# Performance work log

Measured on AMD Instinct MI355X. Metric: run time of the kernel, lower is better.

## Reference

```python
import jax, jax.numpy as jnp
import numpy as np

B, C, L, D, H = 8, 64, 128, 768, 768  # batch, candidates, tokens, hidden, mlp hidden


def setup_inputs() -> dict:
    key = jax.random.key(0)
    k0, k1, k2 = jax.random.split(key, 3)
    inp = jax.random.normal(k0, (B, C, 2, L, D), dtype=jnp.float32)
    # MlpModule params (input_size = 768*2): Linear(2D->H) -> ReLU -> Linear(H->1)
    W1 = jax.random.normal(k1, (2 * D, H), dtype=jnp.float32) * 0.02
    b1 = jnp.zeros((H,), dtype=jnp.float32)
    W2 = jax.random.normal(k2, (H, 1), dtype=jnp.float32) * 0.02
    b2 = jnp.zeros((1,), dtype=jnp.float32)
    return {"input": inp, "W1": W1, "b1": b1, "W2": W2, "b2": b2}


def reference(input, W1, b1, W2, b2):
    b, c, _, l, d = input.shape
    context = input[:, :, 0].reshape(b * c, l, d)  # [BC, L, D]
    entity = input[:, :, 1].reshape(b * c, l, d)   # [BC, L, D]
    mask = (context[:, :, 0] != 0).astype(context.dtype)  # [BC, L]

    # bmm similarity: [BC, L, L]
    sim = jnp.einsum('bld,bmd->blm', context, entity)
    dot_scores = jnp.max(sim, axis=-1)          # [BC, L]
    argmax_values = jnp.argmax(sim, axis=-1)    # [BC, L]

    # gather best-matching entity token per context token: [BC, L, D]
    gathered = jnp.take_along_axis(entity, argmax_values[..., None], axis=1)

    # MLP over stacked (context, entity) pair -> flatten to 2D features
    mlp_in = jnp.concatenate([context, gathered], axis=-1)  # [BC, L, 2D]
    h = jax.nn.relu(mlp_in @ W1 + b1)
    scores = (h @ W2 + b2)[..., 0]              # [BC, L]

    scores = jnp.sum(scores * mask, axis=-1)              # [BC]
    dot_scores = jnp.sum(dot_scores * mask, axis=-1).reshape(b, c)  # [B, C]
    return scores, dot_scores
```

## Files before the change

### kernel.cpp

```cpp
#include <hip/hip_runtime.h>
#include <hip/hip_bf16.h>
#include <stdint.h>

#define NPAIR 512
#define LTOK  128
#define DDIM  768
#define HDIM  768
#define K2    1536
#define MARGIN 0.4f

typedef float f32x4 __attribute__((ext_vector_type(4)));
typedef short bf16x8 __attribute__((ext_vector_type(8)));

static __device__ __forceinline__ int fsw(int row) {
    return (row ^ (row >> 2)) & 3;
}

static __device__ __forceinline__ unsigned short f2bf(float f) {
    union { float f; uint32_t u; } v; v.f = f;
    uint32_t u = v.u;
    u += 0x7FFF + ((u >> 16) & 1);
    return (unsigned short)(u >> 16);
}

static __device__ __forceinline__ uint2 pack4(f32x4 v) {
    __hip_bfloat162 lo = __float22bfloat162_rn(float2{v[0], v[1]});
    __hip_bfloat162 hi = __float22bfloat162_rn(float2{v[2], v[3]});
    uint2 r;
    r.x = *reinterpret_cast<unsigned*>(&lo);
    r.y = *reinterpret_cast<unsigned*>(&hi);
    return r;
}

static __device__ __forceinline__ uint4 pack8(f32x4 a, f32x4 b) {
    uint2 lo = pack4(a), hi = pack4(b);
    uint4 r; r.x = lo.x; r.y = lo.y; r.z = hi.x; r.w = hi.y;
    return r;
}

typedef const __attribute__((address_space(1))) void* gas_t;
typedef __attribute__((address_space(3))) void* las_t;
static __device__ __forceinline__ void gld16(const void* g, void* l) {
    __builtin_amdgcn_global_load_lds((gas_t)g, (las_t)l, 16, 0, 0);
}

static __device__ __forceinline__ float wave_dot(const float* __restrict__ a,
                                                 const float* __restrict__ b,
                                                 int lane) {
    f32x4 s4 = {0.f, 0.f, 0.f, 0.f};
#pragma unroll
    for (int it = 0; it < 3; ++it) {
        int k = it * 256 + lane * 4;
        f32x4 av = *(const f32x4*)(a + k);
        f32x4 bv = *(const f32x4*)(b + k);
#pragma unroll
        for (int q = 0; q < 4; ++q) s4[q] = fmaf(av[q], bv[q], s4[q]);
    }
    float v = (s4[0] + s4[1]) + (s4[2] + s4[3]);
#pragma unroll
    for (int m = 1; m < 64; m <<= 1) v += __shfl_xor(v, m);
    return v;
}

__global__ __launch_bounds__(256, 2) void simfma_kernel(
        const float* __restrict__ inp,
        float* __restrict__ dotmax, int* __restrict__ argmax,
        unsigned short* __restrict__ Cbf, unsigned short* __restrict__ Ebf)
{
    const int p    = blockIdx.x;
    const int t    = threadIdx.x;
    const int wv   = t >> 6;
    const int lane = t & 63;
    const int s    = lane & 15, g = lane >> 4;

    const float* Cbase = inp + (size_t)(2 * p) * LTOK * DDIM;
    const float* Ebase = Cbase + (size_t)LTOK * DDIM;

    __shared__ unsigned short Cl[2][128][32];
    __shared__ unsigned short El[2][128][32];
    __shared__ unsigned short cand[128][16];
    __shared__ int   ccnt[128];
    __shared__ float rm1[128];
    __shared__ int   ri1[128];

    if (t < 128) ccnt[t] = 0;

    f32x4 acc[2][8];
#pragma unroll
    for (int i = 0; i < 2; i++)
#pragma unroll
        for (int j = 0; j < 8; j++) acc[i][j] = (f32x4){0.f, 0.f, 0.f, 0.f};

    const int srow[4] = { (0*256 + t) >> 3, (1*256 + t) >> 3,
                          (2*256 + t) >> 3, (3*256 + t) >> 3 };
    const int so8 = t & 7;
    const int sh  = so8 >> 2;
    const int sq  = so8 & 3;

    f32x4 cbuf[8], ebuf[8];

    auto ISSUE = [&](int kc) {
        const int k0 = kc * 64;
#pragma unroll
        for (int it = 0; it < 4; ++it) {
            const float* ca = Cbase + (size_t)srow[it] * DDIM + k0 + so8 * 8;
            const float* ea = Ebase + (size_t)srow[it] * DDIM + k0 + so8 * 8;
            cbuf[it * 2]     = *(const f32x4*)ca;
            cbuf[it * 2 + 1] = *(const f32x4*)(ca + 4);
            ebuf[it * 2]     = *(const f32x4*)ea;
            ebuf[it * 2 + 1] = *(const f32x4*)(ea + 4);
        }
    };

    ISSUE(0);
    for (int kc = 0; kc < 12; ++kc) {
        const int k0 = kc * 64;
        uint4 cw[4], ew[4];
#pragma unroll
        for (int it = 0; it < 4; ++it) {
            cw[it] = pack8(cbuf[it * 2], cbuf[it * 2 + 1]);
            ew[it] = pack8(ebuf[it * 2], ebuf[it * 2 + 1]);
            const int qs = (sq ^ fsw(srow[it])) * 8;
            *(uint4*)&Cl[sh][srow[it]][qs] = cw[it];
            *(uint4*)&El[sh][srow[it]][qs] = ew[it];
        }
        __syncthreads();

        if (kc < 11) ISSUE(kc + 1);
#pragma unroll
        for (int it = 0; it < 4; ++it) {
            size_t off = ((size_t)p * LTOK + srow[it]) * DDIM + k0 + so8 * 8;
            *(uint4*)(Cbf + off) = cw[it];
            *(uint4*)(Ebf + off) = ew[it];
        }

#pragma unroll
        for (int h = 0; h < 2; ++h) {
            bf16x8 af[2], bfr[8];
#pragma unroll
            for (int i = 0; i < 2; ++i) {
                const int row = wv * 32 + i * 16 + s;
                af[i] = *(const bf16x8*)&Cl[h][row][(g ^ fsw(row)) * 8];
            }
#pragma unroll
            for (int j = 0; j < 8; ++j) {
                const int row = j * 16 + s;
                bfr[j] = *(const bf16x8*)&El[h][row][(g ^ fsw(row)) * 8];
            }
#pragma unroll
            for (int i = 0; i < 2; ++i)
#pragma unroll
                for (int j = 0; j < 8; ++j)
                    acc[i][j] = __builtin_amdgcn_mfma_f32_16x16x32_bf16(af[i], bfr[j], acc[i][j], 0, 0, 0);
        }
        __syncthreads();
    }

#pragma unroll
    for (int i = 0; i < 2; ++i)
#pragma unroll
        for (int r = 0; r < 4; ++r) {
            float m1 = acc[i][0][r]; int i1 = s; float m2 = -1e30f;
#pragma unroll
            for (int j = 1; j < 8; ++j) {
                float v = acc[i][j][r]; int c = j * 16 + s;
                if (v > m1 || (v == m1 && c < i1)) { m2 = m1; m1 = v; i1 = c; }
                else if (v > m2) m2 = v;
            }
#pragma unroll
            for (int msk = 1; msk < 16; msk <<= 1) {
                float o1 = __shfl_xor(m1, msk);
                int   oi = __shfl_xor(i1, msk);
                float o2 = __shfl_xor(m2, msk);
                bool take = (o1 > m1) || (o1 == m1 && oi < i1);
                float nm2 = take ? fmaxf(m1, o2) : fmaxf(m2, o1);
                if (take) { m1 = o1; i1 = oi; }
                m2 = nm2;
            }
            int row = wv * 32 + i * 16 + g * 4 + r;
            if (s == 0) { rm1[row] = m1; ri1[row] = i1; }
            float thr = m1 - MARGIN;
#pragma unroll
            for (int j = 0; j < 8; ++j) {
                float v = acc[i][j][r]; int c = j * 16 + s;
                if (v >= thr && c != i1) {
                    int idx = atomicAdd(&ccnt[row], 1);
                    if (idx < 16) cand[row][idx] = (unsigned short)c;
                }
            }
        }
    __syncthreads();

    for (int rr = 0; rr < 32; ++rr) {
        int row = wv + rr * 4;
        int cnt = ccnt[row];
        float m1 = rm1[row]; int i1 = ri1[row];
        size_t ob = (size_t)p * LTOK + row;
        if (cnt == 0) {
            if (lane == 0) { dotmax[ob] = m1; argmax[ob] = i1; }
            continue;
        }
        const float* cr = Cbase + (size_t)row * DDIM;
        float bv; int bc;
        if (cnt <= 16) {
            bv = wave_dot(cr, Ebase + (size_t)i1 * DDIM, lane); bc = i1;
            for (int q = 0; q < cnt; ++q) {
                int c = cand[row][q];
                float v = wave_dot(cr, Ebase + (size_t)c * DDIM, lane);
                if (v > bv || (v == bv && c < bc)) { bv = v; bc = c; }
            }
        } else {
            bv = -1e30f; bc = 0;
            for (int c = 0; c < 128; ++c) {
                float v = wave_dot(cr, Ebase + (size_t)c * DDIM, lane);
                if (v > bv || (v == bv && c < bc)) { bv = v; bc = c; }
            }
        }
        if (lane == 0) { dotmax[ob] = bv; argmax[ob] = bc; }
    }
}

__global__ __launch_bounds__(256) void w1t_kernel(
        const float* __restrict__ W1, unsigned short* __restrict__ W1T)
{
    int idx = blockIdx.x * 256 + threadIdx.x;
    if (idx >= HDIM * K2 / 8) return;
    int c  = idx / (K2 / 8);
    int k0 = (idx % (K2 / 8)) * 8;
    unsigned short v[8];
#pragma unroll
    for (int q = 0; q < 8; q++) v[q] = f2bf(W1[(size_t)(k0 + q) * HDIM + c]);
    *(uint4*)(W1T + (size_t)c * K2 + k0) = *(const uint4*)v;
}

__global__ __launch_bounds__(256, 2) void mlp2_kernel(
        const unsigned short* __restrict__ Cbf,
        const unsigned short* __restrict__ Ebf,
        const unsigned short* __restrict__ W1T,
        const float* __restrict__ b1,
        const float* __restrict__ W2,
        const int* __restrict__ argmax,
        float* __restrict__ part)
{
    const int p    = blockIdx.x;
    const int cbk  = blockIdx.y;
    const int t    = threadIdx.x;
    const int wv   = t >> 6;
    const int lane = t & 63;
    const int s    = lane & 15, g = lane >> 4;
    const int wr   = wv >> 1, wc = wv & 1;

    __shared__ unsigned short Ald[2][128][32];
    __shared__ unsigned short Bld[2][256][32];
    __shared__ int am[128];

    if (t < 128) am[t] = argmax[p * LTOK + t];

    f32x4 acc[4][8];
#pragma unroll
    for (int i = 0; i < 4; i++)
#pragma unroll
        for (int j = 0; j < 8; j++) acc[i][j] = (f32x4){0.f, 0.f, 0.f, 0.f};

    const int rsub = lane >> 2;
    const int chk  = lane & 3;

    auto STAGE = [&](int buf, int kt) {
        const int k0   = kt * 32;
        const bool ctx = (kt < 24);
        const int kloc = ctx ? k0 : (k0 - DDIM);
#pragma unroll
        for (int n = 0; n < 4; ++n) {
            int c0  = (wv * 4 + n) * 16;
            int col = c0 + rsub;
            int ck  = chk ^ fsw(col);
            gld16(W1T + (size_t)(cbk * 256 + col) * K2 + k0 + ck * 8,
                  &Bld[buf][c0][0]);
        }
#pragma unroll
        for (int n = 0; n < 2; ++n) {
            int r0 = (wv * 2 + n) * 16;
            int r  = r0 + rsub;
            int ck = chk ^ fsw(r);
            const unsigned short* base = ctx
                ? (Cbf + ((size_t)p * LTOK + r) * DDIM)
                : (Ebf + ((size_t)p * LTOK + am[r]) * DDIM);
            gld16(base + kloc + ck * 8, &Ald[buf][r0][0]);
        }
    };

    STAGE(0, 0);
    __syncthreads();

    int cur = 0;
    for (int kt = 0; kt < 47; ++kt) {
        STAGE(cur ^ 1, kt + 1);
        bf16x8 af[4], bfr[8];
#pragma unroll
        for (int i = 0; i < 4; ++i) {
            const int row = wr * 64 + i * 16 + s;
            af[i] = *(const bf16x8*)&Ald[cur][row][(g ^ fsw(row)) * 8];
        }
#pragma unroll
        for (int j = 0; j < 8; ++j) {
            const int row = wc * 128 + j * 16 + s;
            bfr[j] = *(const bf16x8*)&Bld[cur][row][(g ^ fsw(row)) * 8];
        }
#pragma unroll
        for (int i = 0; i < 4; ++i)
#pragma unroll
            for (int j = 0; j < 8; ++j)
                acc[i][j] = __builtin_amdgcn_mfma_f32_16x16x32_bf16(af[i], bfr[j], acc[i][j], 0, 0, 0);
        __syncthreads();
        cur ^= 1;
    }
    {
        bf16x8 af[4], bfr[8];
#pragma unroll
        for (int i = 0; i < 4; ++i) {
            const int row = wr * 64 + i * 16 + s;
            af[i] = *(const bf16x8*)&Ald[cur][row][(g ^ fsw(row)) * 8];
        }
#pragma unroll
        for (int j = 0; j < 8; ++j) {
            const int row = wc * 128 + j * 16 + s;
            bfr[j] = *(const bf16x8*)&Bld[cur][row][(g ^ fsw(row)) * 8];
        }
#pragma unroll
        for (int i = 0; i < 4; ++i)
#pragma unroll
            for (int j = 0; j < 8; ++j)
                acc[i][j] = __builtin_amdgcn_mfma_f32_16x16x32_bf16(af[i], bfr[j], acc[i][j], 0, 0, 0);
    }

    float w2v[8], b1v[8];
#pragma unroll
    for (int j = 0; j < 8; j++) {
        int col = cbk * 256 + wc * 128 + j * 16 + s;
        w2v[j] = W2[col];
        b1v[j] = b1[col];
    }
    float ssum[4][4];
#pragma unroll
    for (int i = 0; i < 4; i++)
#pragma unroll
        for (int r = 0; r < 4; r++) ssum[i][r] = 0.f;
#pragma unroll
    for (int i = 0; i < 4; i++)
#pragma unroll
        for (int j = 0; j < 8; j++)
#pragma unroll
            for (int r = 0; r < 4; r++) {
                float h = acc[i][j][r] + b1v[j];
                h = h > 0.f ? h : 0.f;
                ssum[i][r] = fmaf(h, w2v[j], ssum[i][r]);
            }
#pragma unroll
    for (int sft = 1; sft < 16; sft <<= 1)
#pragma unroll
        for (int i = 0; i < 4; i++)
#pragma unroll
            for (int r = 0; r < 4; r++) ssum[i][r] += __shfl_xor(ssum[i][r], sft);
    if (s == 0) {
        const int q = cbk * 2 + wc;
#pragma unroll
        for (int i = 0; i < 4; i++)
#pragma unroll
            for (int r = 0; r < 4; r++)
                part[(size_t)q * (NPAIR * LTOK) + p * LTOK + wr * 64 + i * 16 + g * 4 + r]
                    = ssum[i][r];
    }
}

__global__ __launch_bounds__(128) void reduce6_kernel(
        const float* __restrict__ inp,
        const float* __restrict__ part,
        const float* __restrict__ dotmax,
        const float* __restrict__ b2,
        float* __restrict__ out)
{
    int p = blockIdx.x;
    int l = threadIdx.x;
    float c0  = inp[((size_t)(2 * p) * LTOK + l) * DDIM];
    float msk = (c0 != 0.0f) ? 1.f : 0.f;
    float sc = b2[0];
#pragma unroll
    for (int q = 0; q < 6; ++q)
        sc += part[(size_t)q * (NPAIR * LTOK) + p * LTOK + l];
    sc *= msk;
    float dm = dotmax[p * LTOK + l] * msk;
#pragma unroll
    for (int sh = 1; sh < 64; sh <<= 1) {
        sc += __shfl_xor(sc, sh);
        dm += __shfl_xor(dm, sh);
    }
    __shared__ float tmp[4];
    if ((l & 63) == 0) { tmp[(l >> 6) * 2] = sc; tmp[(l >> 6) * 2 + 1] = dm; }
    __syncthreads();
    if (l == 0) {
        out[p]          = tmp[0] + tmp[2];
        out[NPAIR + p]  = tmp[1] + tmp[3];
    }
}

__global__ __launch_bounds__(256) void sim_fp32_kernel(
        const float* __restrict__ inp,
        float* __restrict__ dotmax, int* __restrict__ argmax)
{
    const int p  = blockIdx.x;
    const int t  = threadIdx.x;
    const int tx = t & 15, ty = t >> 4;
    const float* Cbase = inp + (size_t)(2 * p) * LTOK * DDIM;
    const float* Ebase = Cbase + (size_t)LTOK * DDIM;

    __shared__ float Ct[128][36];
    __shared__ float Et[128][36];

    float acc[8][8];
#pragma unroll
    for (int i = 0; i < 8; i++)
#pragma unroll
        for (int j = 0; j < 8; j++) acc[i][j] = 0.f;

    for (int kc = 0; kc < 24; ++kc) {
        const int k0 = kc * 32;
#pragma unroll
        for (int q = 0; q < 4; ++q) {
            int f = q * 256 + t;
            int row = f >> 3, c4 = f & 7;
            *(f32x4*)&Ct[row][c4 * 4] = *(const f32x4*)(Cbase + (size_t)row * DDIM + k0 + c4 * 4);
            *(f32x4*)&Et[row][c4 * 4] = *(const f32x4*)(Ebase + (size_t)row * DDIM + k0 + c4 * 4);
        }
        __syncthreads();
#pragma unroll
        for (int kk4 = 0; kk4 < 8; ++kk4) {
            f32x4 cr[8], er[8];
#pragma unroll
            for (int i = 0; i < 8; i++) cr[i] = *(const f32x4*)&Ct[ty + 16 * i][kk4 * 4];
#pragma unroll
            for (int j = 0; j < 8; j++) er[j] = *(const f32x4*)&Et[tx + 16 * j][kk4 * 4];
#pragma unroll
            for (int kk = 0; kk < 4; kk++)
#pragma unroll
                for (int i = 0; i < 8; i++)
#pragma unroll
                    for (int j = 0; j < 8; j++)
                        acc[i][j] = fmaf(cr[i][kk], er[j][kk], acc[i][j]);
        }
        __syncthreads();
    }
#pragma unroll
    for (int i = 0; i < 8; i++) {
        float m = acc[i][0]; int mi = tx;
#pragma unroll
        for (int j = 1; j < 8; j++) {
            int c = tx + 16 * j;
            float v = acc[i][j];
            if (v > m || (v == m && c < mi)) { m = v; mi = c; }
        }
#pragma unroll
        for (int sft = 1; sft < 16; sft <<= 1) {
            float vo = __shfl_xor(m, sft);
            int   io = __shfl_xor(mi, sft);
            if (vo > m || (vo == m && io < mi)) { m = vo; mi = io; }
        }
        if (tx == 0) {
            int r = ty + 16 * i;
            dotmax[(size_t)p * LTOK + r] = m;
            argmax[(size_t)p * LTOK + r] = mi;
        }
    }
}

__global__ __launch_bounds__(256, 2) void mlp_kernel(
        const float* __restrict__ inp,
        const unsigned short* __restrict__ W1T,
        const float* __restrict__ b1,
        const float* __restrict__ W2,
        const int* __restrict__ argmax,
        float* __restrict__ tokscore)
{
    const int tile = blockIdx.x;
    const int cb   = blockIdx.y;
    const int t    = threadIdx.x;
    const int wv   = t >> 6;
    const int lane = t & 63;
    const int s    = lane & 15, g = lane >> 4;

    __shared__ unsigned short At[64][32];
    __shared__ unsigned short Bt[384][32];
    __shared__ int am[64];

    if (t < 64) am[t] = argmax[tile * 64 + t];
    __syncthreads();

    f32x4 acc[4][6];
#pragma unroll
    for (int i = 0; i < 4; i++)
#pragma unroll
        for (int j = 0; j < 6; j++) acc[i][j] = (f32x4){0.f, 0.f, 0.f, 0.f};

    for (int kc = 0; kc < 48; ++kc) {
        const int k0  = kc * 32;
        const int sel = (kc >= 24) ? 1 : 0;
        const int kloc = k0 - sel * DDIM;
#pragma unroll
        for (int q = 0; q < 2; ++q) {
            int f = q * 256 + t;
            int row = f >> 3, c4 = f & 7;
            int token = tile * 64 + row;
            int pp = token >> 7;
            int lsel = sel ? am[row] : (token & 127);
            const float* src = inp + ((size_t)(2 * pp + sel) * LTOK + lsel) * DDIM + kloc + c4 * 4;
            f32x4 v = *(const f32x4*)src;
            uint2 pk = pack4(v);
            *(uint2*)&At[row][c4 * 4] = pk;
        }
#pragma unroll
        for (int q = 0; q < 6; ++q) {
            int f = q * 256 + t;
            int colr = f >> 2, q8 = f & 3;
            const unsigned short* src = W1T + (size_t)(cb * 384 + colr) * K2 + k0 + q8 * 8;
            *(uint4*)&Bt[colr][q8 * 8] = *(const uint4*)src;
        }
        __syncthreads();

        bf16x8 af[4], bfr[6];
#pragma unroll
        for (int i = 0; i < 4; i++) af[i]  = *(const bf16x8*)&At[i * 16 + s][g * 8];
#pragma unroll
        for (int j = 0; j < 6; j++) bfr[j] = *(const bf16x8*)&Bt[wv * 96 + j * 16 + s][g * 8];
#pragma unroll
        for (int i = 0; i < 4; i++)
#pragma unroll
            for (int j = 0; j < 6; j++)
                acc[i][j] = __builtin_amdgcn_mfma_f32_16x16x32_bf16(af[i], bfr[j], acc[i][j], 0, 0, 0);
        __syncthreads();
    }

    float w2v[6], b1v[6];
#pragma unroll
    for (int j = 0; j < 6; j++) {
        int col = cb * 384 + wv * 96 + j * 16 + s;
        w2v[j] = W2[col];
        b1v[j] = b1[col];
    }
    float ssum[4][4];
#pragma unroll
    for (int i = 0; i < 4; i++)
#pragma unroll
        for (int r = 0; r < 4; r++) ssum[i][r] = 0.f;
#pragma unroll
    for (int i = 0; i < 4; i++)
#pragma unroll
        for (int j = 0; j < 6; j++)
#pragma unroll
            for (int r = 0; r < 4; r++) {
                float h = acc[i][j][r] + b1v[j];
                h = h > 0.f ? h : 0.f;
                ssum[i][r] = fmaf(h, w2v[j], ssum[i][r]);
            }
#pragma unroll
    for (int sft = 1; sft < 16; sft <<= 1)
#pragma unroll
        for (int i = 0; i < 4; i++)
#pragma unroll
            for (int r = 0; r < 4; r++) ssum[i][r] += __shfl_xor(ssum[i][r], sft);
    if (s == 0) {
#pragma unroll
        for (int i = 0; i < 4; i++)
#pragma unroll
            for (int r = 0; r < 4; r++)
                atomicAdd(&tokscore[tile * 64 + i * 16 + g * 4 + r], ssum[i][r]);
    }
}

__global__ __launch_bounds__(128) void reduce_kernel(
        const float* __restrict__ inp,
        const float* __restrict__ tokscore,
        const float* __restrict__ dotmax,
        const float* __restrict__ b2,
        float* __restrict__ out)
{
    int p = blockIdx.x;
    int l = threadIdx.x;
    float c0  = inp[((size_t)(2 * p) * LTOK + l) * DDIM];
    float msk = (c0 != 0.0f) ? 1.f : 0.f;
    float sc  = (tokscore[p * LTOK + l] + b2[0]) * msk;
    float dm  = dotmax[p * LTOK + l] * msk;
#pragma unroll
    for (int sh = 1; sh < 64; sh <<= 1) {
        sc += __shfl_xor(sc, sh);
        dm += __shfl_xor(dm, sh);
    }
    __shared__ float tmp[4];
    if ((l & 63) == 0) { tmp[(l >> 6) * 2] = sc; tmp[(l >> 6) * 2 + 1] = dm; }
    __syncthreads();
    if (l == 0) {
        out[p]          = tmp[0] + tmp[2];
        out[NPAIR + p]  = tmp[1] + tmp[3];
    }
}

extern "C" void kernel_launch(void* const* d_in, const int* in_sizes, int n_in,
                              void* d_out, int out_size, void* d_ws, size_t ws_size,
                              hipStream_t stream)
{
    const float* inp = (const float*)d_in[0];
    const float* W1  = (const float*)d_in[1];
    const float* b1  = (const float*)d_in[2];
    const float* W2  = (const float*)d_in[3];
    const float* b2  = (const float*)d_in[4];
    float* out = (float*)d_out;

    char* ws = (char*)d_ws;
    unsigned short* W1T   = (unsigned short*)ws;
    float*          dotmx = (float*)(ws + 2359296);
    int*            amax  = (int*)(ws + 2359296 + 262144);
    float*          toksc = (float*)(ws + 2359296 + 2*262144);
    unsigned short* Cbf   = (unsigned short*)(ws + 2359296 + 3*262144);
    unsigned short* Ebf   = Cbf + (size_t)NPAIR * LTOK * DDIM;
    float*          part  = (float*)(ws + 2359296 + 3*262144 + 2*100663296ull);
    const size_t NEED = 2359296ull + 3ull*262144ull + 2ull*100663296ull + 6ull*262144ull;

    const bool big = ws_size >= NEED;

    w1t_kernel<<<(HDIM * K2 / 8 + 255) / 256, 256, 0, stream>>>(W1, W1T);
    if (big) {
        simfma_kernel<<<NPAIR, 256, 0, stream>>>(inp, dotmx, amax, Cbf, Ebf);
        mlp2_kernel<<<dim3(NPAIR, 3), 256, 0, stream>>>(Cbf, Ebf, W1T, b1, W2, amax, part);
        reduce6_kernel<<<NPAIR, 128, 0, stream>>>(inp, part, dotmx, b2, out);
    } else {
        hipMemsetAsync(toksc, 0, 65536 * sizeof(float), stream);
        sim_fp32_kernel<<<NPAIR, 256, 0, stream>>>(inp, dotmx, amax);
        mlp_kernel<<<dim3(1024, 2), 256, 0, stream>>>(inp, W1T, b1, W2, amax, toksc);
        reduce_kernel<<<NPAIR, 128, 0, stream>>>(inp, toksc, dotmx, b2, out);
    }
}
```

Before: 329.3 us.

## Use 512 threads per block in similarity kernel, one 16-row tile per wave

Doubles the similarity kernel's block size from 256 to 512 threads (8 waves). Each wave now owns 16 context rows instead of 32, and each thread stages two rows per k-chunk instead of four. Per-thread accumulators and staging registers are halved, so occupancy can rise with launch bounds (512,4), and the refinement loop is split across 8 waves. The trade-off is less B-fragment reuse per wave: each wave loads the full entity tile for only one A fragment.

```diff
diff --git a/kernel.cpp b/kernel.cpp
--- a/kernel.cpp
+++ b/kernel.cpp
@@ -62,7 +62,7 @@
     return v;
 }
 
-__global__ __launch_bounds__(256, 2) void simfma_kernel(
+__global__ __launch_bounds__(512, 4) void simfma_kernel(
         const float* __restrict__ inp,
         float* __restrict__ dotmax, int* __restrict__ argmax,
         unsigned short* __restrict__ Cbf, unsigned short* __restrict__ Ebf)
@@ -85,114 +85,107 @@
 
     if (t < 128) ccnt[t] = 0;
 
-    f32x4 acc[2][8];
-#pragma unroll
-    for (int i = 0; i < 2; i++)
-#pragma unroll
-        for (int j = 0; j < 8; j++) acc[i][j] = (f32x4){0.f, 0.f, 0.f, 0.f};
-
-    const int srow[4] = { (0*256 + t) >> 3, (1*256 + t) >> 3,
-                          (2*256 + t) >> 3, (3*256 + t) >> 3 };
-    const int so8 = t & 7;
-    const int sh  = so8 >> 2;
-    const int sq  = so8 & 3;
-
-    f32x4 cbuf[8], ebuf[8];
+    f32x4 acc[8];
+#pragma unroll
+    for (int j = 0; j < 8; j++) acc[j] = (f32x4){0.f, 0.f, 0.f, 0.f};
+
+    const int srow0 = t >> 3;
+    const int srow1 = 64 + srow0;
+    const int so8   = t & 7;
+    const int sh    = so8 >> 2;
+    const int sq    = so8 & 3;
+    const int qs0   = (sq ^ fsw(srow0)) * 8;
+    const int qs1   = (sq ^ fsw(srow1)) * 8;
+
+    f32x4 cbuf[4], ebuf[4];
 
     auto ISSUE = [&](int kc) {
         const int k0 = kc * 64;
-#pragma unroll
-        for (int it = 0; it < 4; ++it) {
-            const float* ca = Cbase + (size_t)srow[it] * DDIM + k0 + so8 * 8;
-            const float* ea = Ebase + (size_t)srow[it] * DDIM + k0 + so8 * 8;
-            cbuf[it * 2]     = *(const f32x4*)ca;
-            cbuf[it * 2 + 1] = *(const f32x4*)(ca + 4);
-            ebuf[it * 2]     = *(const f32x4*)ea;
-            ebuf[it * 2 + 1] = *(const f32x4*)(ea + 4);
-        }
+        const float* c0a = Cbase + (size_t)srow0 * DDIM + k0 + so8 * 8;
+        const float* c1a = Cbase + (size_t)srow1 * DDIM + k0 + so8 * 8;
+        const float* e0a = Ebase + (size_t)srow0 * DDIM + k0 + so8 * 8;
+        const float* e1a = Ebase + (size_t)srow1 * DDIM + k0 + so8 * 8;
+        cbuf[0] = *(const f32x4*)c0a;  cbuf[1] = *(const f32x4*)(c0a + 4);
+        cbuf[2] = *(const f32x4*)c1a;  cbuf[3] = *(const f32x4*)(c1a + 4);
+        ebuf[0] = *(const f32x4*)e0a;  ebuf[1] = *(const f32x4*)(e0a + 4);
+        ebuf[2] = *(const f32x4*)e1a;  ebuf[3] = *(const f32x4*)(e1a + 4);
     };
 
     ISSUE(0);
     for (int kc = 0; kc < 12; ++kc) {
         const int k0 = kc * 64;
-        uint4 cw[4], ew[4];
-#pragma unroll
-        for (int it = 0; it < 4; ++it) {
-            cw[it] = pack8(cbuf[it * 2], cbuf[it * 2 + 1]);
-            ew[it] = pack8(ebuf[it * 2], ebuf[it * 2 + 1]);
-            const int qs = (sq ^ fsw(srow[it])) * 8;
-            *(uint4*)&Cl[sh][srow[it]][qs] = cw[it];
-            *(uint4*)&El[sh][srow[it]][qs] = ew[it];
-        }
+        uint4 cw0 = pack8(cbuf[0], cbuf[1]);
+        uint4 cw1 = pack8(cbuf[2], cbuf[3]);
+        uint4 ew0 = pack8(ebuf[0], ebuf[1]);
+        uint4 ew1 = pack8(ebuf[2], ebuf[3]);
+        *(uint4*)&Cl[sh][srow0][qs0] = cw0;
+        *(uint4*)&Cl[sh][srow1][qs1] = cw1;
+        *(uint4*)&El[sh][srow0][qs0] = ew0;
+        *(uint4*)&El[sh][srow1][qs1] = ew1;
         __syncthreads();
 
         if (kc < 11) ISSUE(kc + 1);
-#pragma unroll
-        for (int it = 0; it < 4; ++it) {
-            size_t off = ((size_t)p * LTOK + srow[it]) * DDIM + k0 + so8 * 8;
-            *(uint4*)(Cbf + off) = cw[it];
-            *(uint4*)(Ebf + off) = ew[it];
+        {
+            size_t o0 = ((size_t)p * LTOK + srow0) * DDIM + k0 + so8 * 8;
+            size_t o1 = ((size_t)p * LTOK + srow1) * DDIM + k0 + so8 * 8;
+            *(uint4*)(Cbf + o0) = cw0;
+            *(uint4*)(Cbf + o1) = cw1;
+            *(uint4*)(Ebf + o0) = ew0;
+            *(uint4*)(Ebf + o1) = ew1;
         }
 
 #pragma unroll
         for (int h = 0; h < 2; ++h) {
-            bf16x8 af[2], bfr[8];
-#pragma unroll
-            for (int i = 0; i < 2; ++i) {
-                const int row = wv * 32 + i * 16 + s;
-                af[i] = *(const bf16x8*)&Cl[h][row][(g ^ fsw(row)) * 8];
-            }
+            const int arow = wv * 16 + s;
+            bf16x8 af = *(const bf16x8*)&Cl[h][arow][(g ^ fsw(arow)) * 8];
+            bf16x8 bfr[8];
 #pragma unroll
             for (int j = 0; j < 8; ++j) {
                 const int row = j * 16 + s;
                 bfr[j] = *(const bf16x8*)&El[h][row][(g ^ fsw(row)) * 8];
             }
 #pragma unroll
-            for (int i = 0; i < 2; ++i)
-#pragma unroll
-                for (int j = 0; j < 8; ++j)
-                    acc[i][j] = __builtin_amdgcn_mfma_f32_16x16x32_bf16(af[i], bfr[j], acc[i][j], 0, 0, 0);
+            for (int j = 0; j < 8; ++j)
+                acc[j] = __builtin_amdgcn_mfma_f32_16x16x32_bf16(af, bfr[j], acc[j], 0, 0, 0);
         }
         __syncthreads();
     }
 
 #pragma unroll
-    for (int i = 0; i < 2; ++i)
-#pragma unroll
-        for (int r = 0; r < 4; ++r) {
-            float m1 = acc[i][0][r]; int i1 = s; float m2 = -1e30f;
-#pragma unroll
-            for (int j = 1; j < 8; ++j) {
-                float v = acc[i][j][r]; int c = j * 16 + s;
-                if (v > m1 || (v == m1 && c < i1)) { m2 = m1; m1 = v; i1 = c; }
-                else if (v > m2) m2 = v;
+    for (int r = 0; r < 4; ++r) {
+        float m1 = acc[0][r]; int i1 = s; float m2 = -1e30f;
+#pragma unroll
+        for (int j = 1; j < 8; ++j) {
+            float v = acc[j][r]; int c = j * 16 + s;
+            if (v > m1 || (v == m1 && c < i1)) { m2 = m1; m1 = v; i1 = c; }
+            else if (v > m2) m2 = v;
+        }
+#pragma unroll
+        for (int msk = 1; msk < 16; msk <<= 1) {
+            float o1 = __shfl_xor(m1, msk);
+            int   oi = __shfl_xor(i1, msk);
+            float o2 = __shfl_xor(m2, msk);
+            bool take = (o1 > m1) || (o1 == m1 && oi < i1);
+            float nm2 = take ? fmaxf(m1, o2) : fmaxf(m2, o1);
+            if (take) { m1 = o1; i1 = oi; }
+            m2 = nm2;
+        }
+        int row = wv * 16 + g * 4 + r;
+        if (s == 0) { rm1[row] = m1; ri1[row] = i1; }
+        float thr = m1 - MARGIN;
+#pragma unroll
+        for (int j = 0; j < 8; ++j) {
+            float v = acc[j][r]; int c = j * 16 + s;
+            if (v >= thr && c != i1) {
+                int idx = atomicAdd(&ccnt[row], 1);
+                if (idx < 16) cand[row][idx] = (unsigned short)c;
             }
-#pragma unroll
-            for (int msk = 1; msk < 16; msk <<= 1) {
-                float o1 = __shfl_xor(m1, msk);
-                int   oi = __shfl_xor(i1, msk);
-                float o2 = __shfl_xor(m2, msk);
-                bool take = (o1 > m1) || (o1 == m1 && oi < i1);
-                float nm2 = take ? fmaxf(m1, o2) : fmaxf(m2, o1);
-                if (take) { m1 = o1; i1 = oi; }
-                m2 = nm2;
-            }
-            int row = wv * 32 + i * 16 + g * 4 + r;
-            if (s == 0) { rm1[row] = m1; ri1[row] = i1; }
-            float thr = m1 - MARGIN;
-#pragma unroll
-            for (int j = 0; j < 8; ++j) {
-                float v = acc[i][j][r]; int c = j * 16 + s;
-                if (v >= thr && c != i1) {
-                    int idx = atomicAdd(&ccnt[row], 1);
-                    if (idx < 16) cand[row][idx] = (unsigned short)c;
-                }
-            }
-        }
+        }
+    }
     __syncthreads();
 
-    for (int rr = 0; rr < 32; ++rr) {
-        int row = wv + rr * 4;
+    for (int rr = 0; rr < 16; ++rr) {
+        int row = wv + rr * 8;
         int cnt = ccnt[row];
         float m1 = rm1[row]; int i1 = ri1[row];
         size_t ob = (size_t)p * LTOK + row;
@@ -627,7 +620,7 @@
 
     w1t_kernel<<<(HDIM * K2 / 8 + 255) / 256, 256, 0, stream>>>(W1, W1T);
     if (big) {
-        simfma_kernel<<<NPAIR, 256, 0, stream>>>(inp, dotmx, amax, Cbf, Ebf);
+        simfma_kernel<<<NPAIR, 512, 0, stream>>>(inp, dotmx, amax, Cbf, Ebf);
         mlp2_kernel<<<dim3(NPAIR, 3), 256, 0, stream>>>(Cbf, Ebf, W1T, b1, W2, amax, part);
         reduce6_kernel<<<NPAIR, 128, 0, stream>>>(inp, part, dotmx, b2, out);
     } else {
```

After: 324.2 us. About the same (-1.5%).
